# Kernel tuning notes

Hardware: AMD Instinct MI355X
Metric: run time of the kernel (lower is better)

The kernel has to match this reference:

```python
import jax, jax.numpy as jnp
import numpy as np

B, N, CC, CF, H, W = 4, 4, 256, 512, 128, 128
h, w = H // 2, W // 2


def _upsample2x(x):
    return jnp.repeat(jnp.repeat(x, 2, axis=2), 2, axis=3)


def setup_inputs() -> dict:
    key = jax.random.key(0)
    ks = jax.random.split(key, 8)
    return {
        "contexts": jax.random.normal(ks[0], (B, N, CC, H, W), dtype=jnp.float32),
        "mainstream": jax.random.normal(ks[1], (B, CF, h, w), dtype=jnp.float32),
        "Wc_w": jax.random.normal(ks[2], (CC, CC), dtype=jnp.float32) * 0.02,  # 1x1 conv Cc->Cc
        "Wc_b": jnp.zeros((CC,), dtype=jnp.float32),
        "Wf_w": jax.random.normal(ks[3], (CC, CF), dtype=jnp.float32) * 0.02,  # 1x1 conv Cf->Cc
        "Wf_b": jnp.zeros((CC,), dtype=jnp.float32),
        "Wv_w": jax.random.normal(ks[4], (CC, CF, 3, 3), dtype=jnp.float32) * 0.02,  # 3x3 conv Cf->Cc
        "Wv_b": jnp.zeros((CC,), dtype=jnp.float32),
    }


def reference(contexts, mainstream, Wc_w, Wc_b, Wf_w, Wf_b, Wv_w, Wv_b):
    # queries: 1x1 conv Cf->Cc on mainstream  [B,Cc,h,w]
    queries = jnp.einsum('oc,bchw->bohw', Wf_w, mainstream) + Wf_b[None, :, None, None]
    # keys: 1x1 conv Cc->Cc applied to every context  [B,N,Cc,H,W]
    keys = jnp.einsum('oc,bnchw->bnohw', Wc_w, contexts) + Wc_b[None, None, :, None, None]
    # values: 3x3 conv Cf->Cc, padding 1  [B,Cc,h,w]
    values = jax.lax.conv_general_dilated(
        mainstream, Wv_w, window_strides=(1, 1), padding='SAME',
        dimension_numbers=('NCHW', 'OIHW', 'NCHW')) + Wv_b[None, :, None, None]
    q_up = _upsample2x(queries)   # [B,Cc,H,W]
    v_up = _upsample2x(values)    # [B,Cc,H,W]
    # per-pixel attention scores over the N contexts
    scores = jnp.einsum('bnchw,bchw->bnhw', keys, q_up)      # [B,N,H,W]
    attn = jax.nn.softmax(scores, axis=1)                    # softmax over contexts
    attn_out = jnp.einsum('bnchw,bnhw->bchw', contexts, attn)
    return attn_out + v_up
```

## Files before the change

### kernel.cpp

```cpp
#include <hip/hip_runtime.h>

#define NB   4
#define NN   4
#define CCh  256
#define CFh  512
#define HH   128
#define WW   128
#define PLO  4096
#define PHI  16384

typedef __bf16 bf16;
typedef __bf16 bf16x8 __attribute__((ext_vector_type(8)));
typedef float  f32x4  __attribute__((ext_vector_type(4)));
typedef float  f32x2  __attribute__((ext_vector_type(2)));

__device__ __forceinline__ void gll16(const void* g, void* lds) {
    __builtin_amdgcn_global_load_lds(
        (const __attribute__((address_space(1))) void*)g,
        (__attribute__((address_space(3))) void*)lds, 16, 0, 0);
}

__global__ void prep_mqk(const float* __restrict__ Wc_w, const float* __restrict__ Wf_w,
                         const float* __restrict__ Wf_b, bf16* __restrict__ M_qk,
                         float* __restrict__ d_qk) {
    __shared__ float red[256];
    int c = blockIdx.y;
    int f = blockIdx.x * 256 + threadIdx.x;
    float s = 0.f;
    for (int o = 0; o < CCh; ++o)
        s += Wc_w[o * CCh + c] * Wf_w[o * CFh + f];
    M_qk[c * CFh + f] = (bf16)s;
    if (blockIdx.x == 0) {
        int o = threadIdx.x;
        red[o] = Wc_w[o * CCh + c] * Wf_b[o];
        __syncthreads();
        for (int st = 128; st > 0; st >>= 1) {
            if (threadIdx.x < st) red[threadIdx.x] += red[threadIdx.x + st];
            __syncthreads();
        }
        if (threadIdx.x == 0) d_qk[c] = red[0];
    }
}

__global__ void prep_ms(const float* __restrict__ ms, bf16* __restrict__ ms_t) {
    __shared__ float tile[32][33];
    int b = blockIdx.z;
    int p0 = blockIdx.x * 32, f0 = blockIdx.y * 32;
    int tx = threadIdx.x;
    int r = tx >> 5, cc = tx & 31;
    const float* src = ms + (size_t)b * CFh * PLO;
#pragma unroll
    for (int q = 0; q < 4; ++q) {
        int fl = q * 8 + r;
        tile[fl][cc] = src[(size_t)(f0 + fl) * PLO + p0 + cc];
    }
    __syncthreads();
    bf16* dst = ms_t + (size_t)b * PLO * CFh;
#pragma unroll
    for (int q = 0; q < 4; ++q) {
        int pl = q * 8 + r;
        dst[(size_t)(p0 + pl) * CFh + f0 + cc] = (bf16)tile[cc][pl];
    }
}

__global__ void prep_wv(const float* __restrict__ Wv_w, bf16* __restrict__ Wv_p,
                        bf16* __restrict__ zerob) {
    int tid = blockIdx.x * 256 + threadIdx.x;
    int t = tid / (CCh * CFh);
    int rem = tid % (CCh * CFh);
    int c = rem / CFh, f = rem % CFh;
    Wv_p[tid] = (bf16)Wv_w[(size_t)(c * CFh + f) * 9 + t];
    if (tid < 1024) zerob[tid] = (bf16)0.f;
}

__global__ __launch_bounds__(256) void gemm_kernel(
    const bf16* __restrict__ Wv_p,
    const bf16* __restrict__ M_qk,
    const bf16* __restrict__ ms_t,
    const float* __restrict__ d_qk,
    const float* __restrict__ Wv_b,
    const bf16* __restrict__ zerob,
    float* __restrict__ v_out, bf16* __restrict__ qk_out) {
    __shared__ __align__(16) bf16 Alds[2][128 * 32];
    __shared__ __align__(16) bf16 Blds[2][128 * 32];

    const int tx = threadIdx.x;
    const int wave = tx >> 6, lane = tx & 63;
    const int ptile = blockIdx.x, ctile = blockIdx.y;
    const int z = blockIdx.z;
    const int mode = (z >= 4);
    const int b = mode ? (z - 4) : z;
    const int NIT = mode ? 16 : 144;

    const bf16* Wbase = mode ? M_qk : Wv_p;
    const bf16* msb = ms_t + (size_t)b * PLO * CFh;

    int idx0 = wave * 2048 + lane * 16;
    int idx1 = idx0 + 1024;
    int rA0 = idx0 >> 6, fq0 = (idx0 >> 4) & 3;
    int rA1 = idx1 >> 6, fq1 = (idx1 >> 4) & 3;
    const size_t aoff0 = (size_t)(ctile * 128 + rA0) * CFh + fq0 * 8;
    const size_t aoff1 = (size_t)(ctile * 128 + rA1) * CFh + fq1 * 8;

    const int p0 = ptile * 128 + rA0, p1 = ptile * 128 + rA1;
    const int i0_ = p0 >> 6, j0_ = p0 & 63;
    const int i1_ = p1 >> 6, j1_ = p1 & 63;

    f32x4 acc[4][4];
#pragma unroll
    for (int mi = 0; mi < 4; ++mi)
#pragma unroll
        for (int ni = 0; ni < 4; ++ni) acc[mi][ni] = f32x4{0.f, 0.f, 0.f, 0.f};

    const int wm = wave >> 1, wn = wave & 1;
    const int quad = lane >> 4, l15 = lane & 15;

    const bf16* bs0c; const bf16* bs1c; const bf16* Wtc;
#define SET_TAP(tt) do {                                                        \
        int t_ = (tt);                                                          \
        int dy = mode ? 0 : (t_ / 3 - 1);                                       \
        int dx = mode ? 0 : (t_ % 3 - 1);                                       \
        int si0 = i0_ + dy, sj0 = j0_ + dx;                                     \
        int si1 = i1_ + dy, sj1 = j1_ + dx;                                     \
        bs0c = ((unsigned)si0 < 64u && (unsigned)sj0 < 64u)                     \
                   ? msb + (size_t)(si0 * 64 + sj0) * CFh + fq0 * 8 : zerob;    \
        bs1c = ((unsigned)si1 < 64u && (unsigned)sj1 < 64u)                     \
                   ? msb + (size_t)(si1 * 64 + sj1) * CFh + fq1 * 8 : zerob;    \
        Wtc = Wbase + (size_t)t_ * CCh * CFh;                                   \
    } while (0)

    SET_TAP(0);
    {
        char* lA = (char*)(&Alds[0][0]) + wave * 2048;
        char* lB = (char*)(&Blds[0][0]) + wave * 2048;
        gll16(Wtc + aoff0, lA);
        gll16(Wtc + aoff1, lA + 1024);
        gll16(bs0c, lB);
        gll16(bs1c, lB + 1024);
    }
    __syncthreads();

    for (int it = 0; it < NIT; ++it) {
        const int buf = it & 1;
        const int nx = it + 1;
        if (nx < NIT) {
            if ((nx & 15) == 0) SET_TAP(nx >> 4);
            const int f0 = (nx & 15) * 32;
            char* lA = (char*)(&Alds[buf ^ 1][0]) + wave * 2048;
            char* lB = (char*)(&Blds[buf ^ 1][0]) + wave * 2048;
            gll16(Wtc + aoff0 + f0, lA);
            gll16(Wtc + aoff1 + f0, lA + 1024);
            gll16(bs0c + f0, lB);
            gll16(bs1c + f0, lB + 1024);
        }
        const bf16* Ab = &Alds[buf][0];
        const bf16* Bb = &Blds[buf][0];
        bf16x8 af[4], bfr[4];
#pragma unroll
        for (int mi = 0; mi < 4; ++mi)
            af[mi] = *(const bf16x8*)&Ab[(wm * 64 + mi * 16 + l15) * 32 + quad * 8];
#pragma unroll
        for (int ni = 0; ni < 4; ++ni)
            bfr[ni] = *(const bf16x8*)&Bb[(wn * 64 + ni * 16 + l15) * 32 + quad * 8];
#pragma unroll
        for (int mi = 0; mi < 4; ++mi)
#pragma unroll
            for (int ni = 0; ni < 4; ++ni)
                acc[mi][ni] = __builtin_amdgcn_mfma_f32_16x16x32_bf16(
                    af[mi], bfr[ni], acc[mi][ni], 0, 0, 0);
        __syncthreads();
    }
#undef SET_TAP

    if (mode) {
        bf16* obase = qk_out + (size_t)b * CCh * PLO;
#pragma unroll
        for (int mi = 0; mi < 4; ++mi) {
            int cb = ctile * 128 + wm * 64 + mi * 16 + quad * 4;
#pragma unroll
            for (int ni = 0; ni < 4; ++ni) {
                int p = ptile * 128 + wn * 64 + ni * 16 + l15;
                bf16* op = obase + (size_t)cb * PLO + p;
#pragma unroll
                for (int r = 0; r < 4; ++r)
                    op[(size_t)r * PLO] = (bf16)(acc[mi][ni][r] + d_qk[cb + r]);
            }
        }
    } else {
        float* obase = v_out + (size_t)b * CCh * PLO;
#pragma unroll
        for (int mi = 0; mi < 4; ++mi) {
            int cb = ctile * 128 + wm * 64 + mi * 16 + quad * 4;
#pragma unroll
            for (int ni = 0; ni < 4; ++ni) {
                int p = ptile * 128 + wn * 64 + ni * 16 + l15;
                float* op = obase + (size_t)cb * PLO + p;
#pragma unroll
                for (int r = 0; r < 4; ++r)
                    op[(size_t)r * PLO] = acc[mi][ni][r] + Wv_b[cb + r];
            }
        }
    }
}

__global__ __launch_bounds__(512, 4) void attn_kernel(
    const float* __restrict__ ctx,
    const bf16* __restrict__ qk,
    const float* __restrict__ v,
    float* __restrict__ out) {
    __shared__ f32x2 swred[4][8][16];
    const int tx = threadIdx.x;
    const int pq = tx & 15;
    const int cc = tx >> 4;
    const int lane = tx & 63;
    const int wv = tx >> 6;
    const int quad = lane >> 4;

    const int pbase = blockIdx.x << 5;
    const int b = pbase >> 14;
    const int rem = pbase & 16383;
    const int hh = rem >> 7;
    const int w0 = rem & 127;
    const int wq = w0 + pq * 2;
    const int i = hh >> 1, j = wq >> 1;

    const int c0 = cc * 8;
    const size_t NSTR = (size_t)CCh * PHI;
    const float* cbase = ctx + (size_t)b * NN * NSTR + (size_t)c0 * PHI
                             + (size_t)hh * WW + wq;
    const bf16* qkb = qk + ((size_t)b * CCh + c0) * PLO + i * 64 + j;
    const float* vbp = v + ((size_t)b * CCh + c0) * PLO + i * 64 + j;

    f32x2 vals[4][8];
    f32x2 s[4];
#pragma unroll
    for (int n = 0; n < 4; ++n) s[n] = f32x2{0.f, 0.f};

#pragma unroll
    for (int cj = 0; cj < 8; ++cj) {
        float q = (float)qkb[(size_t)cj * PLO];
        f32x2 qv = {q, q};
#pragma unroll
        for (int n = 0; n < 4; ++n) {
            vals[n][cj] = *(const f32x2*)(cbase + n * NSTR + (size_t)cj * PHI);
            s[n] += vals[n][cj] * qv;
        }
    }
#pragma unroll
    for (int n = 0; n < 4; ++n) {
#pragma unroll
        for (int m = 16; m <= 32; m <<= 1) {
            f32x2 t;
            t[0] = __shfl_xor(s[n][0], m);
            t[1] = __shfl_xor(s[n][1], m);
            s[n] += t;
        }
    }
    f32x2 sq = (quad == 0) ? s[0] : (quad == 1) ? s[1] : (quad == 2) ? s[2] : s[3];
    swred[quad][wv][pq] = sq;
    __syncthreads();

    f32x2 t4[4];
#pragma unroll
    for (int n = 0; n < 4; ++n) {
        f32x2 a = swred[n][0][pq];
#pragma unroll
        for (int w = 1; w < 8; ++w) a += swred[n][w][pq];
        t4[n] = a;
    }
    f32x2 mx;
#pragma unroll
    for (int k = 0; k < 2; ++k)
        mx[k] = fmaxf(fmaxf(t4[0][k], t4[1][k]), fmaxf(t4[2][k], t4[3][k]));
    f32x2 e[4];
#pragma unroll
    for (int n = 0; n < 4; ++n)
#pragma unroll
        for (int k = 0; k < 2; ++k) e[n][k] = __expf(t4[n][k] - mx[k]);
    f32x2 ssum = e[0] + e[1] + e[2] + e[3];
    f32x2 rs;
    rs[0] = 1.f / ssum[0];
    rs[1] = 1.f / ssum[1];
    f32x2 a4[4];
#pragma unroll
    for (int n = 0; n < 4; ++n) a4[n] = e[n] * rs;

    float* outp = out + ((size_t)b * CCh + c0) * PHI + (size_t)hh * WW + wq;
#pragma unroll
    for (int cj = 0; cj < 8; ++cj) {
        float vvv = vbp[(size_t)cj * PLO];
        f32x2 o = vals[0][cj] * a4[0] + vals[1][cj] * a4[1] +
                  vals[2][cj] * a4[2] + vals[3][cj] * a4[3] +
                  f32x2{vvv, vvv};
        *(f32x2*)(outp + (size_t)cj * PHI) = o;
    }
}

extern "C" void kernel_launch(void* const* d_in, const int* in_sizes, int n_in,
                              void* d_out, int out_size, void* d_ws, size_t ws_size,
                              hipStream_t stream) {
    const float* ctx  = (const float*)d_in[0];
    const float* ms   = (const float*)d_in[1];
    const float* Wc_w = (const float*)d_in[2];
    const float* Wf_w = (const float*)d_in[4];
    const float* Wf_b = (const float*)d_in[5];
    const float* Wv_w = (const float*)d_in[6];
    const float* Wv_b = (const float*)d_in[7];
    float* out = (float*)d_out;

    char* ws = (char*)d_ws;
    bf16*  ms_t  = (bf16*)ws;
    bf16*  Wv_p  = (bf16*)(ws + 16777216);
    bf16*  M_qk  = (bf16*)(ws + 19136512);
    float* d_qk  = (float*)(ws + 19398656);
    bf16*  zerob = (bf16*)(ws + 19399680);
    bf16*  qk    = (bf16*)(ws + 19401728);
    float* v     = (float*)(ws + 27790336);

    prep_mqk<<<dim3(2, 256), 256, 0, stream>>>(Wc_w, Wf_w, Wf_b, M_qk, d_qk);
    prep_ms<<<dim3(128, 16, 4), 256, 0, stream>>>(ms, ms_t);
    prep_wv<<<dim3(4608), 256, 0, stream>>>(Wv_w, Wv_p, zerob);
    gemm_kernel<<<dim3(32, 2, 8), 256, 0, stream>>>(Wv_p, M_qk, ms_t, d_qk,
                                                    Wv_b, zerob, v, qk);
    attn_kernel<<<dim3(2048), 512, 0, stream>>>(ctx, qk, v, out);
}
```

Measured before the change: 535.8 us.

## Halve GEMM pixel tile to 64 and widen attention loads to float4

The GEMM kernel's pixel tile shrinks from 128 to 64, exactly one image row, which doubles the grid to 1024 blocks. This gives more parallelism on the many-CU GPU and simplifies the per-tap halo address computation, at the cost of less reuse of each loaded weight tile. The attention kernel now handles 4 pixels and 4 channels per thread with 16-byte context loads and stores, unpacks two bf16 q values from one 32-bit word, and reads v as a float2. The cross-lane reduction gains one shuffle stage to compensate.

```diff
diff --git a/kernel.cpp b/kernel.cpp
--- a/kernel.cpp
+++ b/kernel.cpp
@@ -82,7 +82,7 @@
     const bf16* __restrict__ zerob,
     float* __restrict__ v_out, bf16* __restrict__ qk_out) {
     __shared__ __align__(16) bf16 Alds[2][128 * 32];
-    __shared__ __align__(16) bf16 Blds[2][128 * 32];
+    __shared__ __align__(16) bf16 Blds[2][64 * 32];
 
     const int tx = threadIdx.x;
     const int wave = tx >> 6, lane = tx & 63;
@@ -101,42 +101,36 @@
     int rA1 = idx1 >> 6, fq1 = (idx1 >> 4) & 3;
     const size_t aoff0 = (size_t)(ctile * 128 + rA0) * CFh + fq0 * 8;
     const size_t aoff1 = (size_t)(ctile * 128 + rA1) * CFh + fq1 * 8;
-
-    const int p0 = ptile * 128 + rA0, p1 = ptile * 128 + rA1;
-    const int i0_ = p0 >> 6, j0_ = p0 & 63;
-    const int i1_ = p1 >> 6, j1_ = p1 & 63;
-
-    f32x4 acc[4][4];
+    const int rB = wave * 16 + (lane >> 2);
+    const int fqB = lane & 3;
+
+    f32x4 acc[4][2];
 #pragma unroll
     for (int mi = 0; mi < 4; ++mi)
 #pragma unroll
-        for (int ni = 0; ni < 4; ++ni) acc[mi][ni] = f32x4{0.f, 0.f, 0.f, 0.f};
+        for (int ni = 0; ni < 2; ++ni) acc[mi][ni] = f32x4{0.f, 0.f, 0.f, 0.f};
 
     const int wm = wave >> 1, wn = wave & 1;
     const int quad = lane >> 4, l15 = lane & 15;
 
-    const bf16* bs0c; const bf16* bs1c; const bf16* Wtc;
+    const bf16* bsC; const bf16* Wtc;
 #define SET_TAP(tt) do {                                                        \
         int t_ = (tt);                                                          \
         int dy = mode ? 0 : (t_ / 3 - 1);                                       \
         int dx = mode ? 0 : (t_ % 3 - 1);                                       \
-        int si0 = i0_ + dy, sj0 = j0_ + dx;                                     \
-        int si1 = i1_ + dy, sj1 = j1_ + dx;                                     \
-        bs0c = ((unsigned)si0 < 64u && (unsigned)sj0 < 64u)                     \
-                   ? msb + (size_t)(si0 * 64 + sj0) * CFh + fq0 * 8 : zerob;    \
-        bs1c = ((unsigned)si1 < 64u && (unsigned)sj1 < 64u)                     \
-                   ? msb + (size_t)(si1 * 64 + sj1) * CFh + fq1 * 8 : zerob;    \
+        int si = ptile + dy, sj = rB + dx;                                      \
+        bsC = ((unsigned)si < 64u && (unsigned)sj < 64u)                        \
+                  ? msb + (size_t)(si * 64 + sj) * CFh + fqB * 8 : zerob;       \
         Wtc = Wbase + (size_t)t_ * CCh * CFh;                                   \
     } while (0)
 
     SET_TAP(0);
     {
         char* lA = (char*)(&Alds[0][0]) + wave * 2048;
-        char* lB = (char*)(&Blds[0][0]) + wave * 2048;
+        char* lB = (char*)(&Blds[0][0]) + wave * 1024;
         gll16(Wtc + aoff0, lA);
         gll16(Wtc + aoff1, lA + 1024);
-        gll16(bs0c, lB);
-        gll16(bs1c, lB + 1024);
+        gll16(bsC, lB);
     }
     __syncthreads();
 
@@ -147,25 +141,24 @@
             if ((nx & 15) == 0) SET_TAP(nx >> 4);
             const int f0 = (nx & 15) * 32;
             char* lA = (char*)(&Alds[buf ^ 1][0]) + wave * 2048;
-            char* lB = (char*)(&Blds[buf ^ 1][0]) + wave * 2048;
+            char* lB = (char*)(&Blds[buf ^ 1][0]) + wave * 1024;
             gll16(Wtc + aoff0 + f0, lA);
             gll16(Wtc + aoff1 + f0, lA + 1024);
-            gll16(bs0c + f0, lB);
-            gll16(bs1c + f0, lB + 1024);
+            gll16(bsC + f0, lB);
         }
         const bf16* Ab = &Alds[buf][0];
         const bf16* Bb = &Blds[buf][0];
-        bf16x8 af[4], bfr[4];
+        bf16x8 af[4], bfr[2];
 #pragma unroll
         for (int mi = 0; mi < 4; ++mi)
             af[mi] = *(const bf16x8*)&Ab[(wm * 64 + mi * 16 + l15) * 32 + quad * 8];
 #pragma unroll
-        for (int ni = 0; ni < 4; ++ni)
-            bfr[ni] = *(const bf16x8*)&Bb[(wn * 64 + ni * 16 + l15) * 32 + quad * 8];
+        for (int ni = 0; ni < 2; ++ni)
+            bfr[ni] = *(const bf16x8*)&Bb[(wn * 32 + ni * 16 + l15) * 32 + quad * 8];
 #pragma unroll
         for (int mi = 0; mi < 4; ++mi)
 #pragma unroll
-            for (int ni = 0; ni < 4; ++ni)
+            for (int ni = 0; ni < 2; ++ni)
                 acc[mi][ni] = __builtin_amdgcn_mfma_f32_16x16x32_bf16(
                     af[mi], bfr[ni], acc[mi][ni], 0, 0, 0);
         __syncthreads();
@@ -178,8 +171,8 @@
         for (int mi = 0; mi < 4; ++mi) {
             int cb = ctile * 128 + wm * 64 + mi * 16 + quad * 4;
 #pragma unroll
-            for (int ni = 0; ni < 4; ++ni) {
-                int p = ptile * 128 + wn * 64 + ni * 16 + l15;
+            for (int ni = 0; ni < 2; ++ni) {
+                int p = ptile * 64 + wn * 32 + ni * 16 + l15;
                 bf16* op = obase + (size_t)cb * PLO + p;
 #pragma unroll
                 for (int r = 0; r < 4; ++r)
@@ -192,8 +185,8 @@
         for (int mi = 0; mi < 4; ++mi) {
             int cb = ctile * 128 + wm * 64 + mi * 16 + quad * 4;
 #pragma unroll
-            for (int ni = 0; ni < 4; ++ni) {
-                int p = ptile * 128 + wn * 64 + ni * 16 + l15;
+            for (int ni = 0; ni < 2; ++ni) {
+                int p = ptile * 64 + wn * 32 + ni * 16 + l15;
                 float* op = obase + (size_t)cb * PLO + p;
 #pragma unroll
                 for (int r = 0; r < 4; ++r)
@@ -208,91 +201,96 @@
     const bf16* __restrict__ qk,
     const float* __restrict__ v,
     float* __restrict__ out) {
-    __shared__ f32x2 swred[4][8][16];
+    __shared__ f32x4 swred[4][8][8];
     const int tx = threadIdx.x;
-    const int pq = tx & 15;
-    const int cc = tx >> 4;
+    const int pq = tx & 7;
+    const int cc = tx >> 3;
     const int lane = tx & 63;
     const int wv = tx >> 6;
-    const int quad = lane >> 4;
+    const int g = lane >> 3;
 
     const int pbase = blockIdx.x << 5;
     const int b = pbase >> 14;
     const int rem = pbase & 16383;
     const int hh = rem >> 7;
     const int w0 = rem & 127;
-    const int wq = w0 + pq * 2;
-    const int i = hh >> 1, j = wq >> 1;
-
-    const int c0 = cc * 8;
+    const int wq = w0 + pq * 4;
+    const int i = hh >> 1, j0 = wq >> 1;
+
+    const int c0 = cc * 4;
     const size_t NSTR = (size_t)CCh * PHI;
     const float* cbase = ctx + (size_t)b * NN * NSTR + (size_t)c0 * PHI
                              + (size_t)hh * WW + wq;
-    const bf16* qkb = qk + ((size_t)b * CCh + c0) * PLO + i * 64 + j;
-    const float* vbp = v + ((size_t)b * CCh + c0) * PLO + i * 64 + j;
-
-    f32x2 vals[4][8];
-    f32x2 s[4];
-#pragma unroll
-    for (int n = 0; n < 4; ++n) s[n] = f32x2{0.f, 0.f};
-
-#pragma unroll
-    for (int cj = 0; cj < 8; ++cj) {
-        float q = (float)qkb[(size_t)cj * PLO];
-        f32x2 qv = {q, q};
+    const bf16* qkb = qk + ((size_t)b * CCh + c0) * PLO + i * 64 + j0;
+    const float* vbp = v + ((size_t)b * CCh + c0) * PLO + i * 64 + j0;
+
+    f32x4 vals[4][4];
+    f32x4 s[4];
+#pragma unroll
+    for (int n = 0; n < 4; ++n) s[n] = f32x4{0.f, 0.f, 0.f, 0.f};
+
+#pragma unroll
+    for (int cj = 0; cj < 4; ++cj) {
+        unsigned qw = *(const unsigned*)(qkb + (size_t)cj * PLO);
+        float qa = __uint_as_float(qw << 16);
+        float qb = __uint_as_float(qw & 0xffff0000u);
+        f32x4 qv = {qa, qa, qb, qb};
 #pragma unroll
         for (int n = 0; n < 4; ++n) {
-            vals[n][cj] = *(const f32x2*)(cbase + n * NSTR + (size_t)cj * PHI);
+            vals[n][cj] = *(const f32x4*)(cbase + n * NSTR + (size_t)cj * PHI);
             s[n] += vals[n][cj] * qv;
         }
     }
 #pragma unroll
     for (int n = 0; n < 4; ++n) {
 #pragma unroll
-        for (int m = 16; m <= 32; m <<= 1) {
-            f32x2 t;
+        for (int m = 8; m <= 32; m <<= 1) {
+            f32x4 t;
             t[0] = __shfl_xor(s[n][0], m);
             t[1] = __shfl_xor(s[n][1], m);
+            t[2] = __shfl_xor(s[n][2], m);
+            t[3] = __shfl_xor(s[n][3], m);
             s[n] += t;
         }
     }
-    f32x2 sq = (quad == 0) ? s[0] : (quad == 1) ? s[1] : (quad == 2) ? s[2] : s[3];
-    swred[quad][wv][pq] = sq;
+    f32x4 sq = (g == 0 || g == 4) ? s[0] : (g == 1 || g == 5) ? s[1]
+             : (g == 2 || g == 6) ? s[2] : s[3];
+    if (g < 4) swred[g][wv][pq] = sq;
     __syncthreads();
 
-    f32x2 t4[4];
+    f32x4 t4[4];
 #pragma unroll
     for (int n = 0; n < 4; ++n) {
-        f32x2 a = swred[n][0][pq];
+        f32x4 a = swred[n][0][pq];
 #pragma unroll
         for (int w = 1; w < 8; ++w) a += swred[n][w][pq];
         t4[n] = a;
     }
-    f32x2 mx;
-#pragma unroll
-    for (int k = 0; k < 2; ++k)
+    f32x4 mx;
+#pragma unroll
+    for (int k = 0; k < 4; ++k)
         mx[k] = fmaxf(fmaxf(t4[0][k], t4[1][k]), fmaxf(t4[2][k], t4[3][k]));
-    f32x2 e[4];
+    f32x4 e[4];
 #pragma unroll
     for (int n = 0; n < 4; ++n)
 #pragma unroll
-        for (int k = 0; k < 2; ++k) e[n][k] = __expf(t4[n][k] - mx[k]);
-    f32x2 ssum = e[0] + e[1] + e[2] + e[3];
-    f32x2 rs;
-    rs[0] = 1.f / ssum[0];
-    rs[1] = 1.f / ssum[1];
-    f32x2 a4[4];
+        for (int k = 0; k < 4; ++k) e[n][k] = __expf(t4[n][k] - mx[k]);
+    f32x4 ssum = e[0] + e[1] + e[2] + e[3];
+    f32x4 rs;
+#pragma unroll
+    for (int k = 0; k < 4; ++k) rs[k] = 1.f / ssum[k];
+    f32x4 a4[4];
 #pragma unroll
     for (int n = 0; n < 4; ++n) a4[n] = e[n] * rs;
 
     float* outp = out + ((size_t)b * CCh + c0) * PHI + (size_t)hh * WW + wq;
 #pragma unroll
-    for (int cj = 0; cj < 8; ++cj) {
-        float vvv = vbp[(size_t)cj * PLO];
-        f32x2 o = vals[0][cj] * a4[0] + vals[1][cj] * a4[1] +
+    for (int cj = 0; cj < 4; ++cj) {
+        f32x2 vv = *(const f32x2*)(vbp + (size_t)cj * PLO);
+        f32x4 o = vals[0][cj] * a4[0] + vals[1][cj] * a4[1] +
                   vals[2][cj] * a4[2] + vals[3][cj] * a4[3] +
-                  f32x2{vvv, vvv};
-        *(f32x2*)(outp + (size_t)cj * PHI) = o;
+                  f32x4{vv[0], vv[0], vv[1], vv[1]};
+        *(f32x4*)(outp + (size_t)cj * PHI) = o;
     }
 }
 
@@ -320,7 +318,7 @@
     prep_mqk<<<dim3(2, 256), 256, 0, stream>>>(Wc_w, Wf_w, Wf_b, M_qk, d_qk);
     prep_ms<<<dim3(128, 16, 4), 256, 0, stream>>>(ms, ms_t);
     prep_wv<<<dim3(4608), 256, 0, stream>>>(Wv_w, Wv_p, zerob);
-    gemm_kernel<<<dim3(32, 2, 8), 256, 0, stream>>>(Wv_p, M_qk, ms_t, d_qk,
+    gemm_kernel<<<dim3(64, 2, 8), 256, 0, stream>>>(Wv_p, M_qk, ms_t, d_qk,
                                                     Wv_b, zerob, v, qk);
     attn_kernel<<<dim3(2048), 512, 0, stream>>>(ctx, qk, v, out);
 }
```

After: 527.8 us. No clear change (-1.5%).
